# Performance work log

Measured on AMD Instinct MI355X. Metric: run time of the kernel, lower is better.

## Reference

```python
import jax, jax.numpy as jnp
import numpy as np

B, S, D, H = 4, 2048, 256, 8
HD = D // H
SCALE = float(np.sqrt(HD))  # temperature = head_dim ** 0.5


def setup_inputs() -> dict:
    key = jax.random.key(0)
    ks = jax.random.split(key, 12)
    w = lambda k, shape: jax.random.normal(k, shape, dtype=jnp.float32) * 0.05
    x = jax.random.normal(ks[0], (B, S, D), dtype=jnp.float32)
    adj = jax.random.randint(ks[1], (B, S, S), 0, 2, dtype=jnp.int32)
    return {
        "x": x,
        "adj": adj,
        "w_qkv": w(ks[2], (3 * D, D)),
        "b_qkv": jnp.zeros((3 * D,), jnp.float32),
        "ln_g": jnp.ones((D,), jnp.float32),
        "ln_b": jnp.zeros((D,), jnp.float32),
        "w_fc": w(ks[3], (D, D)),
        "b_fc": jnp.zeros((D,), jnp.float32),
        "w_z": w(ks[4], (D, D)),
        "b_z": jnp.full((D,), -2.0, jnp.float32),  # init_bias fills w_z bias with -2
        "u_z": w(ks[5], (D, D)),
        "w_r": w(ks[6], (D, D)),
        "u_r": w(ks[7], (D, D)),
        "w_g": w(ks[8], (D, D)),
        "u_g": w(ks[9], (D, D)),
    }


def reference(x, adj, w_qkv, b_qkv, ln_g, ln_b, w_fc, b_fc,
              w_z, b_z, u_z, w_r, u_r, w_g, u_g):
    residual = x
    # LayerNorm (eps=1e-5, torch default)
    mu = jnp.mean(x, axis=-1, keepdims=True)
    var = jnp.var(x, axis=-1, keepdims=True)
    xn = (x - mu) / jnp.sqrt(var + 1e-5) * ln_g + ln_b
    # fused QKV projection -> (B*H, S, 3*HD), batch-major over (b, h)
    qkv = xn @ w_qkv.T + b_qkv                       # [B,S,3D]
    qkv = qkv.reshape(B, S, H, 3 * HD).transpose(0, 2, 1, 3).reshape(B * H, S, 3 * HD)
    q, k, v = jnp.split(qkv, 3, axis=-1)
    # masked scaled dot-product attention (full NxN scores, as in original)
    attn = jnp.einsum('nqd,nkd->nqk', q, k) / SCALE  # [B*H,S,S]
    adj_r = jnp.repeat(adj, H, axis=0)               # batch-major, matches attn layout
    attn = jnp.where(adj_r == 0, -jnp.inf, attn)
    attn = jax.nn.softmax(attn, axis=-1)
    out = jnp.einsum('nqk,nkd->nqd', attn, v)        # [B*H,S,HD]
    # Faithful replication of torch's view(n_head, batch, ...) applied to
    # batch-major data (an ordering quirk in the original module).
    out = out.reshape(H, B, S, HD).transpose(1, 2, 0, 3).reshape(B, S, D)
    y = jax.nn.relu(out @ w_fc.T + b_fc)
    # GRU gate: x=residual, y=attention branch
    z = jax.nn.sigmoid(y @ w_z.T + b_z + residual @ u_z.T)
    r = jax.nn.sigmoid(y @ w_r.T + residual @ u_r.T)
    h_hat = jnp.tanh(y @ w_g.T + (r * residual) @ u_g.T)
    return (1.0 - z) * residual + z * h_hat
```

## Files before the change

kernel.cpp:

```cpp
#include <hip/hip_runtime.h>
#include <hip/hip_bf16.h>
#include <math.h>

#define B_  4
#define S_  2048
#define D_  256
#define H_  8
#define HD_ 32
#define QSCALE 0.25504175929589786f

typedef short  bf16x8 __attribute__((ext_vector_type(8)));
typedef float  f32x4  __attribute__((ext_vector_type(4)));
typedef float  f32x16 __attribute__((ext_vector_type(16)));
typedef unsigned short ushort_t;
typedef unsigned int   uint_t;

__device__ __forceinline__ ushort_t f2b(float f) {
    union { float f; unsigned u; } v; v.f = f;
    unsigned r = (v.u + 0x7FFFu + ((v.u >> 16) & 1u)) >> 16;
    return (ushort_t)r;
}
__device__ __forceinline__ float b2f(ushort_t s) {
    return __uint_as_float((uint_t)s << 16);
}
__device__ __forceinline__ f32x16 zero16() {
    f32x16 z;
#pragma unroll
    for (int i = 0; i < 16; ++i) z[i] = 0.f;
    return z;
}

__device__ __forceinline__ float wave_sum(float v) {
#pragma unroll
    for (int o = 32; o > 0; o >>= 1) v += __shfl_down(v, o, 64);
    return v;
}
__device__ __forceinline__ float block_sum256(float v, float* scr) {
    v = wave_sum(v);
    int lane = threadIdx.x & 63, wid = threadIdx.x >> 6;
    if (lane == 0) scr[wid] = v;
    __syncthreads();
    float r = scr[0] + scr[1] + scr[2] + scr[3];
    __syncthreads();
    return r;
}

#define WQ_SZ 196608
#define WS_SZ 65536
#define NB_ADJ 8192
#define NB_WC  2560
#define NB_LN  8192
__global__ __launch_bounds__(256)
void prep_kernel(const int* __restrict__ adj, uint_t* __restrict__ bits,
                 const float* __restrict__ w0, const float* __restrict__ w1,
                 const float* __restrict__ w2, const float* __restrict__ w3,
                 const float* __restrict__ w4, const float* __restrict__ w5,
                 const float* __restrict__ w6, const float* __restrict__ w7,
                 ushort_t* __restrict__ wout,
                 const float* __restrict__ x, const float* __restrict__ g,
                 const float* __restrict__ bb, ushort_t* __restrict__ xn_b) {
    __shared__ float scr[4];
    int blk = blockIdx.x, tid = threadIdx.x;
    if (blk < NB_ADJ) {
        int lane = tid & 63;
        int b = blk >> 11, q = blk & 2047;
        uint_t* outp = bits + ((size_t)b * 64) * 2048 + q;
#pragma unroll
        for (int gp = 0; gp < 8; ++gp) {
            size_t i = ((size_t)blk * 8 + gp) * 256 + tid;
            unsigned long long m = __ballot(adj[i] != 0);
            int w = gp * 8 + ((tid & ~63) >> 5);
            if (lane == 0)  outp[(size_t)w * 2048]       = (uint_t)m;
            if (lane == 32) outp[(size_t)(w + 1) * 2048] = (uint_t)(m >> 32);
        }
    } else if (blk < NB_ADJ + NB_WC) {
        int idx = (blk - NB_ADJ) * 256 + tid;
        const float* src; int o;
        if (idx < WQ_SZ) { src = w0; o = idx; }
        else {
            int j = idx - WQ_SZ, seg = j >> 16; o = j & (WS_SZ - 1);
            src = (seg == 0) ? w1 : (seg == 1) ? w2 : (seg == 2) ? w3 :
                  (seg == 3) ? w4 : (seg == 4) ? w5 : (seg == 5) ? w6 : w7;
        }
        int j  = o & 7;
        int l  = (o >> 3) & 15;
        int qd = (o >> 7) & 3;
        int ks = (o >> 9) & 7;
        int ct = o >> 12;
        wout[idx] = f2b(src[(ct * 16 + l) * 256 + ks * 32 + qd * 8 + j]);
    } else {
        size_t base = (size_t)(blk - NB_ADJ - NB_WC) * D_;
        float v  = x[base + tid];
        float mu = block_sum256(v, scr) * (1.0f / D_);
        float d  = v - mu;
        float var = block_sum256(d * d, scr) * (1.0f / D_);
        float rstd = rsqrtf(var + 1e-5f);
        xn_b[base + tid] = f2b(d * rstd * g[tid] + bb[tid]);
    }
}

__global__ __launch_bounds__(256)
void gemm_qkv(const ushort_t* __restrict__ A, const ushort_t* __restrict__ Wf,
              const float* __restrict__ bias, ushort_t* __restrict__ outb,
              ushort_t* __restrict__ vT, ushort_t* __restrict__ kD) {
    __shared__ ushort_t Sa[64][264];
    int tid = threadIdx.x;
    int wave = tid >> 6, lane = tid & 63, l = lane & 15, quad = lane >> 4;
    int wm = wave >> 1, wn = wave & 1;
    int m0 = blockIdx.y * 64, n0 = blockIdx.x * 64;
    {
#pragma unroll
        for (int j = 0; j < 8; ++j) {
            int u = tid + j * 256;
            int row = u >> 5, c = (u & 31) * 8;
            *(uint4*)&Sa[row][c] = *(const uint4*)(A + (size_t)(m0 + row) * 256 + c);
        }
    }
    __syncthreads();

    bf16x8 af[2][8];
#pragma unroll
    for (int mt = 0; mt < 2; ++mt)
#pragma unroll
        for (int ks = 0; ks < 8; ++ks)
            af[mt][ks] = *(const bf16x8*)&Sa[wm * 32 + mt * 16 + l][ks * 32 + quad * 8];

    f32x4 acc[2][2];
#pragma unroll
    for (int i = 0; i < 2; ++i)
#pragma unroll
        for (int j = 0; j < 2; ++j) acc[i][j] = (f32x4){0.f, 0.f, 0.f, 0.f};

#pragma unroll
    for (int nt = 0; nt < 2; ++nt) {
        int ct = (n0 >> 4) + wn * 2 + nt;
        bf16x8 wfr[8];
#pragma unroll
        for (int ks = 0; ks < 8; ++ks)
            wfr[ks] = *(const bf16x8*)(Wf + (((size_t)ct * 8 + ks) * 64 + lane) * 8);
#pragma unroll
        for (int ks = 0; ks < 8; ++ks) {
            acc[0][nt] = __builtin_amdgcn_mfma_f32_16x16x32_bf16(af[0][ks], wfr[ks], acc[0][nt], 0, 0, 0);
            acc[1][nt] = __builtin_amdgcn_mfma_f32_16x16x32_bf16(af[1][ks], wfr[ks], acc[1][nt], 0, 0, 0);
        }
    }

    __syncthreads();
    ushort_t* So = &Sa[0][0];
#pragma unroll
    for (int nt = 0; nt < 2; ++nt) {
        int col = wn * 32 + nt * 16 + l;
        int gcol = n0 + col;
        float bv = bias[gcol];
        float qs = ((gcol % 96) < 32) ? QSCALE : 1.0f;
#pragma unroll
        for (int mt = 0; mt < 2; ++mt)
#pragma unroll
            for (int r = 0; r < 4; ++r) {
                int row = wm * 32 + mt * 16 + quad * 4 + r;
                So[row * 72 + col] = f2b((acc[mt][nt][r] + bv) * qs);
            }
    }
    __syncthreads();
    {
        int row = tid >> 2, seg = tid & 3;
        uint4 v0 = *(uint4*)&So[row * 72 + seg * 16];
        uint4 v1 = *(uint4*)&So[row * 72 + seg * 16 + 8];
        ushort_t* op = outb + (size_t)(m0 + row) * 768 + n0 + seg * 16;
        ((uint4*)op)[0] = v0;
        ((uint4*)op)[1] = v1;
    }

    int vs = n0 % 96;

    if (vs != 64) {
        int kloc = (vs == 0) ? 32 : 0;
        int h  = (vs == 0) ? (n0 / 96) : ((n0 - 32) / 96);
        int b  = m0 >> 11;
        int s0 = m0 & (S_ - 1);
        int krow = tid >> 2, kd = (tid & 3) * 8;
        uint4 v = *(uint4*)&So[krow * 72 + kloc + kd];
        *(uint4*)&kD[((size_t)(b * 8 + h) * S_ + s0 + krow) * 32 + kd] = v;
    }

    if (vs != 0) {
        int vloc = (vs == 64) ? 0 : 32;
        int h  = (n0 + vloc) / 96;
        int b  = m0 >> 11;
        int s0 = m0 & (S_ - 1);
        ushort_t* vstage = &Sa[0][0] + 8192;
        {
            int c = tid & 31, seg = tid >> 5;
            ushort_t tmp[8];
#pragma unroll
            for (int i = 0; i < 8; ++i)
                tmp[i] = So[(seg * 8 + i) * 72 + vloc + c];
            uint_t u[4];
#pragma unroll
            for (int i = 0; i < 4; ++i)
                u[i] = (uint_t)tmp[2 * i] | ((uint_t)tmp[2 * i + 1] << 16);
            *(uint4*)&vstage[c * 72 + seg * 8] = make_uint4(u[0], u[1], u[2], u[3]);
        }
        __syncthreads();
        {
            int d = tid >> 3, tseg = tid & 7;
            uint4 v = *(uint4*)&vstage[d * 72 + tseg * 8];
            *(uint4*)&vT[((size_t)(b * 8 + h) * 32 + d) * S_ + s0 + tseg * 8] = v;
        }
    }
}

__global__ __launch_bounds__(512)
void fused_gate(const ushort_t* __restrict__ attn_b, const float* __restrict__ xf,
                const ushort_t* __restrict__ wfc, const ushort_t* __restrict__ wz,
                const ushort_t* __restrict__ uz, const ushort_t* __restrict__ wr,
                const ushort_t* __restrict__ ur, const ushort_t* __restrict__ wg,
                const ushort_t* __restrict__ ug, const float* __restrict__ bfc,
                const float* __restrict__ bz, float* __restrict__ out) {
    __shared__ ushort_t Sa[16][264];
    __shared__ ushort_t Sx[16][264];
    __shared__ ushort_t Sy[16][264];
    __shared__ ushort_t St[16][264];
    int tid = threadIdx.x;
    int wave = tid >> 6, lane = tid & 63, l = lane & 15, quad = lane >> 4;
    int m0 = blockIdx.x * 16;
    int colbase = wave * 32;

    {
        int row = tid >> 5, c0 = (tid & 31) * 8;
        const ushort_t* ap = attn_b + (size_t)(m0 + row) * 256 + c0;
        *(uint4*)&Sa[row][c0] = *((const uint4*)ap);
        const float4* xp = (const float4*)(xf + (size_t)(m0 + row) * 256 + c0);
        float4 f0 = xp[0], f1 = xp[1];
        union { __hip_bfloat162 h[4]; uint4 u; } p0;
        p0.h[0] = __float22bfloat162_rn(make_float2(f0.x, f0.y));
        p0.h[1] = __float22bfloat162_rn(make_float2(f0.z, f0.w));
        p0.h[2] = __float22bfloat162_rn(make_float2(f1.x, f1.y));
        p0.h[3] = __float22bfloat162_rn(make_float2(f1.z, f1.w));
        *(uint4*)&Sx[row][c0] = p0.u;
    }
    __syncthreads();

    {
        bf16x8 af[8];
#pragma unroll
        for (int ks = 0; ks < 8; ++ks)
            af[ks] = *(const bf16x8*)&Sa[l][ks * 32 + quad * 8];
        f32x4 ya[2];
#pragma unroll
        for (int nt = 0; nt < 2; ++nt) ya[nt] = (f32x4){0.f, 0.f, 0.f, 0.f};
#pragma unroll
        for (int nt = 0; nt < 2; ++nt) {
            size_t fb = ((size_t)(wave * 2 + nt) * 8) * 512 + lane * 8;
#pragma unroll
            for (int ks = 0; ks < 8; ++ks) {
                bf16x8 wfr = *(const bf16x8*)(wfc + fb + ks * 512);
                ya[nt] = __builtin_amdgcn_mfma_f32_16x16x32_bf16(af[ks], wfr, ya[nt], 0, 0, 0);
            }
        }
#pragma unroll
        for (int nt = 0; nt < 2; ++nt) {
            int col = colbase + nt * 16 + l;
            float bv = bfc[col];
#pragma unroll
            for (int r = 0; r < 4; ++r)
                Sy[quad * 4 + r][col] = f2b(fmaxf(ya[nt][r] + bv, 0.0f));
        }
    }
    __syncthreads();

    f32x4 az[2], ar[2], ag[2];
#pragma unroll
    for (int nt = 0; nt < 2; ++nt) {
        az[nt] = (f32x4){0.f, 0.f, 0.f, 0.f};
        ar[nt] = (f32x4){0.f, 0.f, 0.f, 0.f};
        ag[nt] = (f32x4){0.f, 0.f, 0.f, 0.f};
    }
#pragma unroll
    for (int nt = 0; nt < 2; ++nt) {
        size_t fb = ((size_t)(wave * 2 + nt) * 8) * 512 + lane * 8;
#pragma unroll
        for (int ks = 0; ks < 8; ++ks) {
            bf16x8 fy = *(const bf16x8*)&Sy[l][ks * 32 + quad * 8];
            bf16x8 fx = *(const bf16x8*)&Sx[l][ks * 32 + quad * 8];
            bf16x8 fz  = *(const bf16x8*)(wz + fb + ks * 512);
            bf16x8 fuz = *(const bf16x8*)(uz + fb + ks * 512);
            bf16x8 fr  = *(const bf16x8*)(wr + fb + ks * 512);
            bf16x8 fur = *(const bf16x8*)(ur + fb + ks * 512);
            bf16x8 fg  = *(const bf16x8*)(wg + fb + ks * 512);
            az[nt] = __builtin_amdgcn_mfma_f32_16x16x32_bf16(fy, fz,  az[nt], 0, 0, 0);
            az[nt] = __builtin_amdgcn_mfma_f32_16x16x32_bf16(fx, fuz, az[nt], 0, 0, 0);
            ar[nt] = __builtin_amdgcn_mfma_f32_16x16x32_bf16(fy, fr,  ar[nt], 0, 0, 0);
            ar[nt] = __builtin_amdgcn_mfma_f32_16x16x32_bf16(fx, fur, ar[nt], 0, 0, 0);
            ag[nt] = __builtin_amdgcn_mfma_f32_16x16x32_bf16(fy, fg,  ag[nt], 0, 0, 0);
        }
    }
#pragma unroll
    for (int nt = 0; nt < 2; ++nt) {
        int col = colbase + nt * 16 + l;
        float bzv = bz[col];
#pragma unroll
        for (int r = 0; r < 4; ++r) {
            int row = quad * 4 + r;
            az[nt][r] = 1.0f / (1.0f + __expf(-(az[nt][r] + bzv)));
            float rr  = 1.0f / (1.0f + __expf(-ar[nt][r]));
            St[row][col] = f2b(rr * b2f(Sx[row][col]));
        }
    }
    __syncthreads();

    f32x4 fcc[2];
#pragma unroll
    for (int nt = 0; nt < 2; ++nt) fcc[nt] = (f32x4){0.f, 0.f, 0.f, 0.f};
#pragma unroll
    for (int nt = 0; nt < 2; ++nt) {
        size_t fb = ((size_t)(wave * 2 + nt) * 8) * 512 + lane * 8;
#pragma unroll
        for (int ks = 0; ks < 8; ++ks) {
            bf16x8 ft = *(const bf16x8*)&St[l][ks * 32 + quad * 8];
            bf16x8 fu = *(const bf16x8*)(ug + fb + ks * 512);
            fcc[nt] = __builtin_amdgcn_mfma_f32_16x16x32_bf16(ft, fu, fcc[nt], 0, 0, 0);
        }
    }
#pragma unroll
    for (int nt = 0; nt < 2; ++nt) {
        int col = colbase + nt * 16 + l;
#pragma unroll
        for (int r = 0; r < 4; ++r) {
            int row = quad * 4 + r;
            float v = ag[nt][r] + fcc[nt][r];
            float e = __expf(2.0f * v);
            float h = 1.0f - 2.0f / (e + 1.0f);
            float zz = az[nt][r];
            size_t idx = (size_t)(m0 + row) * 256 + col;
            out[idx] = (1.0f - zz) * xf[idx] + zz * h;
        }
    }
}

__global__ __launch_bounds__(256)
void attn_kernel(const ushort_t* __restrict__ qkvb, const ushort_t* __restrict__ kD,
                 const ushort_t* __restrict__ vT,
                 const uint_t* __restrict__ abits, ushort_t* __restrict__ attn_b) {
    __shared__ ushort_t Ks[2][128][40];
    __shared__ ushort_t Vt[2][32][136];

    int tid = threadIdx.x;
    int wave = tid >> 6, lane = tid & 63;
    int lane5 = lane & 31, hi = lane >> 5;
    int hsh8 = hi * 8;
    int pair = wave >> 1, half = wave & 1;

    int lid = blockIdx.y * 32 + blockIdx.x;
    int L   = (lid & 7) * 128 + (lid >> 3);
    int q0  = (L & 31) * 64;
    int n   = L >> 5;
    int b = n >> 3, h = n & 7;
    int bp = n & 3, hp = n >> 2;

    const ushort_t* base = qkvb + (size_t)b * S_ * 768 + h * 96;
    int qbase = pair * 32;
    int myq = q0 + qbase + lane5;
    const int kofs = half * 64;

    bf16x8 qf1 = *(const bf16x8*)(base + (size_t)myq * 768 + hsh8);
    bf16x8 qf2 = *(const bf16x8*)(base + (size_t)myq * 768 + 16 + hsh8);

    bf16x8 ones;
#pragma unroll
    for (int i = 0; i < 8; ++i) ones[i] = (short)0x3F80;

    f32x16 oacc = zero16(), aones = zero16();

    int skey = tid >> 1, sj = tid & 1;
    int prow = (skey & ~12) | ((skey & 4) << 1) | ((skey & 8) >> 1);
    int pxor = ((prow >> 3) & 1) << 3;
    int vd = tid >> 3, vk = (tid & 7) * 8;
    const ushort_t* vptr = vT + ((size_t)n * 32 + vd) * S_ + vk;
    const ushort_t* kpt  = kD + ((size_t)n * S_ + skey) * 32 + sj * 16;
    const uint_t* tb = abits + ((size_t)b * 64) * 2048 + myq;

    uint_t aw0 = tb[(size_t)(half * 2 + 0) * 2048];
    uint_t aw1 = tb[(size_t)(half * 2 + 1) * 2048];
    {
        uint4 ka = *(const uint4*)(kpt);
        uint4 kb_ = *(const uint4*)(kpt + 8);
        uint4 va = *(const uint4*)(vptr);
        uint4 vb_ = *(const uint4*)(vptr + 64);
        *(uint4*)&Ks[0][prow][(sj * 16 + 0) ^ pxor] = ka;
        *(uint4*)&Ks[0][prow][(sj * 16 + 8) ^ pxor] = kb_;
        *(uint4*)&Vt[0][vd][vk] = va;
        *(uint4*)&Vt[0][vd][vk + 64] = vb_;
    }
    uint4 kv0 = *(const uint4*)(kpt + (size_t)128 * 32);
    uint4 kv1 = *(const uint4*)(kpt + (size_t)128 * 32 + 8);
    uint4 vv0 = *(const uint4*)(vptr + 128);
    uint4 vv1 = *(const uint4*)(vptr + 192);
    __syncthreads();

    int b3 = (lane >> 3) & 1;

    for (int k0 = 0; k0 < S_; k0 += 128) {
        int cur = (k0 >> 7) & 1;
        bool more = (k0 + 128 < S_);
        uint_t awn0, awn1;
        if (more) {
            *(uint4*)&Ks[cur ^ 1][prow][(sj * 16 + 0) ^ pxor] = kv0;
            *(uint4*)&Ks[cur ^ 1][prow][(sj * 16 + 8) ^ pxor] = kv1;
            *(uint4*)&Vt[cur ^ 1][vd][vk] = vv0;
            *(uint4*)&Vt[cur ^ 1][vd][vk + 64] = vv1;
            int wn = ((k0 + 128) >> 5) + half * 2;
            awn0 = tb[(size_t)(wn + 0) * 2048];
            awn1 = tb[(size_t)(wn + 1) * 2048];
            if (k0 + 256 < S_) {
                kv0 = *(const uint4*)(kpt + (size_t)(k0 + 256) * 32);
                kv1 = *(const uint4*)(kpt + (size_t)(k0 + 256) * 32 + 8);
                vv0 = *(const uint4*)(vptr + k0 + 256);
                vv1 = *(const uint4*)(vptr + k0 + 320);
            }
        }

#pragma unroll
        for (int kb2 = 0; kb2 < 2; ++kb2) {
            const int kb = kofs + kb2 * 32;
            bf16x8 kf1 = *(const bf16x8*)&Ks[cur][kb + lane5][(hi ^ b3) * 8];
            bf16x8 kf2 = *(const bf16x8*)&Ks[cur][kb + lane5][((2 + hi) ^ b3) * 8];
            f32x16 sc = zero16();
            sc = __builtin_amdgcn_mfma_f32_32x32x16_bf16(kf1, qf1, sc, 0, 0, 0);
            sc = __builtin_amdgcn_mfma_f32_32x32x16_bf16(kf2, qf2, sc, 0, 0, 0);

            uint_t wsub = (kb2 ? aw1 : aw0) >> hsh8;
            union { uint_t u[8]; bf16x8 v[2]; } pp;
#pragma unroll
            for (int i = 0; i < 8; ++i) {
                const int c = 2 * i + ((i >> 2) * 8);
                float e0 = __builtin_amdgcn_exp2f(sc[2 * i]);
                float e1 = __builtin_amdgcn_exp2f(sc[2 * i + 1]);
                uint_t m0 = (uint_t)((int)(wsub << (31 - c)) >> 31);
                uint_t m1 = (uint_t)((int)(wsub << (30 - c)) >> 31);
                e0 = __uint_as_float(__float_as_uint(e0) & m0);
                e1 = __uint_as_float(__float_as_uint(e1) & m1);
                union { __hip_bfloat162 b2; uint_t u; } p;
                p.b2 = __float22bfloat162_rn(make_float2(e0, e1));
                pp.u[i] = p.u;
            }

            bf16x8 vb1 = *(const bf16x8*)&Vt[cur][lane5][kb + hsh8];
            bf16x8 vb2 = *(const bf16x8*)&Vt[cur][lane5][kb + 16 + hsh8];

            __builtin_amdgcn_s_setprio(1);
            oacc  = __builtin_amdgcn_mfma_f32_32x32x16_bf16(pp.v[0], vb1,  oacc,  0, 0, 0);
            aones = __builtin_amdgcn_mfma_f32_32x32x16_bf16(pp.v[0], ones, aones, 0, 0, 0);
            oacc  = __builtin_amdgcn_mfma_f32_32x32x16_bf16(pp.v[1], vb2,  oacc,  0, 0, 0);
            aones = __builtin_amdgcn_mfma_f32_32x32x16_bf16(pp.v[1], ones, aones, 0, 0, 0);
            __builtin_amdgcn_s_setprio(0);
        }

        if (more) { aw0 = awn0; aw1 = awn1; }
        __syncthreads();
    }

    float* red = (float*)&Ks[0][0][0];
    if (half) {
        float* dst = red + pair * 2048 + lane * 4;
#pragma unroll
        for (int j = 0; j < 4; ++j) {
            f32x4 t;
            t[0] = oacc[4 * j]; t[1] = oacc[4 * j + 1];
            t[2] = oacc[4 * j + 2]; t[3] = oacc[4 * j + 3];
            *(f32x4*)(dst + j * 256) = t;
        }
#pragma unroll
        for (int j = 0; j < 4; ++j) {
            f32x4 t;
            t[0] = aones[4 * j]; t[1] = aones[4 * j + 1];
            t[2] = aones[4 * j + 2]; t[3] = aones[4 * j + 3];
            *(f32x4*)(dst + (4 + j) * 256) = t;
        }
    }
    __syncthreads();
    if (!half) {
        const float* src = red + pair * 2048 + lane * 4;
#pragma unroll
        for (int j = 0; j < 4; ++j) {
            f32x4 t = *(const f32x4*)(src + j * 256);
            oacc[4 * j] += t[0]; oacc[4 * j + 1] += t[1];
            oacc[4 * j + 2] += t[2]; oacc[4 * j + 3] += t[3];
        }
#pragma unroll
        for (int j = 0; j < 4; ++j) {
            f32x4 t = *(const f32x4*)(src + (4 + j) * 256);
            aones[4 * j] += t[0]; aones[4 * j + 1] += t[1];
            aones[4 * j + 2] += t[2]; aones[4 * j + 3] += t[3];
        }
    }
    __syncthreads();

    ushort_t* Ost = &Ks[0][0][0];
    if (!half) {
#pragma unroll
        for (int r = 0; r < 16; ++r) {
            int qr = (r & 3) + 8 * (r >> 2) + 4 * hi;
            Ost[(qbase + qr) * 40 + lane5] = f2b(oacc[r] / aones[r]);
        }
    }
    __syncthreads();
    {
        int row = tid >> 2, part = tid & 3;
        uint4 v = *(uint4*)&Ost[row * 40 + part * 8];
        *(uint4*)&attn_b[((size_t)(bp * S_ + q0 + row)) * 256 + hp * 32 + part * 8] = v;
    }
}

extern "C" void kernel_launch(void* const* d_in, const int* in_sizes, int n_in,
                              void* d_out, int out_size, void* d_ws, size_t ws_size,
                              hipStream_t stream) {
    const float* x     = (const float*)d_in[0];
    const int*   adj   = (const int*)d_in[1];
    const float* w_qkv = (const float*)d_in[2];
    const float* b_qkv = (const float*)d_in[3];
    const float* ln_g  = (const float*)d_in[4];
    const float* ln_b  = (const float*)d_in[5];
    const float* w_fc  = (const float*)d_in[6];
    const float* b_fc  = (const float*)d_in[7];
    const float* w_z   = (const float*)d_in[8];
    const float* b_z   = (const float*)d_in[9];
    const float* u_z   = (const float*)d_in[10];
    const float* w_r   = (const float*)d_in[11];
    const float* u_r   = (const float*)d_in[12];
    const float* w_g   = (const float*)d_in[13];
    const float* u_g   = (const float*)d_in[14];
    float* out = (float*)d_out;

    const size_t TOK  = (size_t)B_ * S_;
    const size_t TOKD = TOK * D_;
    ushort_t* xn_b   = (ushort_t*)d_ws;
    ushort_t* qkv_b  = xn_b + TOKD;
    ushort_t* attn_b = qkv_b + TOK * 768;
    ushort_t* wb     = attn_b + TOKD;
    uint_t*   bits   = (uint_t*)(wb + WQ_SZ + 7 * WS_SZ);
    ushort_t* vTb    = (ushort_t*)(bits + (size_t)B_ * S_ * S_ / 32);
    ushort_t* kDb    = vTb + (size_t)32 * 32 * S_;

    ushort_t* wq_b  = wb;
    ushort_t* wfc_b = wb + WQ_SZ;
    ushort_t* wz_b  = wfc_b + WS_SZ;
    ushort_t* uz_b  = wz_b + WS_SZ;
    ushort_t* wr_b  = uz_b + WS_SZ;
    ushort_t* ur_b  = wr_b + WS_SZ;
    ushort_t* wg_b  = ur_b + WS_SZ;
    ushort_t* ug_b  = wg_b + WS_SZ;

    prep_kernel<<<NB_ADJ + NB_WC + NB_LN, 256, 0, stream>>>(
        adj, bits, w_qkv, w_fc, w_z, u_z, w_r, u_r, w_g, u_g, wb,
        x, ln_g, ln_b, xn_b);

    gemm_qkv<<<dim3(12, 128), 256, 0, stream>>>(xn_b, wq_b, b_qkv, qkv_b, vTb, kDb);

    attn_kernel<<<dim3(S_ / 64, B_ * H_), 256, 0, stream>>>(qkv_b, kDb, vTb, bits, attn_b);

    fused_gate<<<512, 512, 0, stream>>>(
        attn_b, x, wfc_b, wz_b, uz_b, wr_b, ur_b, wg_b, ug_b, b_fc, b_z, out);
}
```

Baseline: 223.6 us.

## Overlap adjacency bitpacking with QKV GEMM and rework LayerNorm and attention loop

Moves the adjacency-to-bitmask packing out of the prep kernel and interleaves it with the QKV GEMM blocks (16 adj blocks per 3 GEMM tiles in one launch), so the bandwidth-bound adj read runs alongside the compute-bound GEMM. LayerNorm now handles one row per wave with float4 loads and xor-shuffle reductions, which removes the shared-memory block reductions and the syncs that went with them. The attention main loop is restructured into 15 unconditional iterations plus a peeled final compute step, with prefetch addresses wrapped to drop the branches. The peeled loop issues one redundant, wrapped prefetch, and the GEMM tiles now depend on the new block interleave mapping.

```diff
diff --git a/kernel.cpp b/kernel.cpp
--- a/kernel.cpp
+++ b/kernel.cpp
@@ -29,52 +29,27 @@
     for (int i = 0; i < 16; ++i) z[i] = 0.f;
     return z;
 }
-
-__device__ __forceinline__ float wave_sum(float v) {
-#pragma unroll
-    for (int o = 32; o > 0; o >>= 1) v += __shfl_down(v, o, 64);
+__device__ __forceinline__ float wave_allsum(float v) {
+#pragma unroll
+    for (int o = 32; o > 0; o >>= 1) v += __shfl_xor(v, o, 64);
     return v;
-}
-__device__ __forceinline__ float block_sum256(float v, float* scr) {
-    v = wave_sum(v);
-    int lane = threadIdx.x & 63, wid = threadIdx.x >> 6;
-    if (lane == 0) scr[wid] = v;
-    __syncthreads();
-    float r = scr[0] + scr[1] + scr[2] + scr[3];
-    __syncthreads();
-    return r;
 }
 
 #define WQ_SZ 196608
 #define WS_SZ 65536
-#define NB_ADJ 8192
 #define NB_WC  2560
-#define NB_LN  8192
+#define NB_LN4 2048
 __global__ __launch_bounds__(256)
-void prep_kernel(const int* __restrict__ adj, uint_t* __restrict__ bits,
-                 const float* __restrict__ w0, const float* __restrict__ w1,
+void prep_kernel(const float* __restrict__ w0, const float* __restrict__ w1,
                  const float* __restrict__ w2, const float* __restrict__ w3,
                  const float* __restrict__ w4, const float* __restrict__ w5,
                  const float* __restrict__ w6, const float* __restrict__ w7,
                  ushort_t* __restrict__ wout,
                  const float* __restrict__ x, const float* __restrict__ g,
                  const float* __restrict__ bb, ushort_t* __restrict__ xn_b) {
-    __shared__ float scr[4];
     int blk = blockIdx.x, tid = threadIdx.x;
-    if (blk < NB_ADJ) {
-        int lane = tid & 63;
-        int b = blk >> 11, q = blk & 2047;
-        uint_t* outp = bits + ((size_t)b * 64) * 2048 + q;
-#pragma unroll
-        for (int gp = 0; gp < 8; ++gp) {
-            size_t i = ((size_t)blk * 8 + gp) * 256 + tid;
-            unsigned long long m = __ballot(adj[i] != 0);
-            int w = gp * 8 + ((tid & ~63) >> 5);
-            if (lane == 0)  outp[(size_t)w * 2048]       = (uint_t)m;
-            if (lane == 32) outp[(size_t)(w + 1) * 2048] = (uint_t)(m >> 32);
-        }
-    } else if (blk < NB_ADJ + NB_WC) {
-        int idx = (blk - NB_ADJ) * 256 + tid;
+    if (blk < NB_WC) {
+        int idx = blk * 256 + tid;
         const float* src; int o;
         if (idx < WQ_SZ) { src = w0; o = idx; }
         else {
@@ -89,25 +64,54 @@
         int ct = o >> 12;
         wout[idx] = f2b(src[(ct * 16 + l) * 256 + ks * 32 + qd * 8 + j]);
     } else {
-        size_t base = (size_t)(blk - NB_ADJ - NB_WC) * D_;
-        float v  = x[base + tid];
-        float mu = block_sum256(v, scr) * (1.0f / D_);
-        float d  = v - mu;
-        float var = block_sum256(d * d, scr) * (1.0f / D_);
-        float rstd = rsqrtf(var + 1e-5f);
-        xn_b[base + tid] = f2b(d * rstd * g[tid] + bb[tid]);
+        int wave = tid >> 6, lane = tid & 63;
+        int row = (blk - NB_WC) * 4 + wave;
+        int col = lane * 4;
+        float4 t = *(const float4*)(x + (size_t)row * 256 + col);
+        float s = wave_allsum(t.x + t.y + t.z + t.w);
+        float mu = s * (1.0f / D_);
+        float d0 = t.x - mu, d1 = t.y - mu, d2 = t.z - mu, d3 = t.w - mu;
+        float v = wave_allsum(d0 * d0 + d1 * d1 + d2 * d2 + d3 * d3);
+        float rstd = rsqrtf(v * (1.0f / D_) + 1e-5f);
+        float4 gv = *(const float4*)(g + col);
+        float4 bv = *(const float4*)(bb + col);
+        union { ushort_t u[4]; uint2 q; } o;
+        o.u[0] = f2b(d0 * rstd * gv.x + bv.x);
+        o.u[1] = f2b(d1 * rstd * gv.y + bv.y);
+        o.u[2] = f2b(d2 * rstd * gv.z + bv.z);
+        o.u[3] = f2b(d3 * rstd * gv.w + bv.w);
+        *(uint2*)(xn_b + (size_t)row * 256 + col) = o.q;
     }
 }
 
 __global__ __launch_bounds__(256)
 void gemm_qkv(const ushort_t* __restrict__ A, const ushort_t* __restrict__ Wf,
               const float* __restrict__ bias, ushort_t* __restrict__ outb,
-              ushort_t* __restrict__ vT, ushort_t* __restrict__ kD) {
+              ushort_t* __restrict__ vT, ushort_t* __restrict__ kD,
+              const int* __restrict__ adj, uint_t* __restrict__ bits) {
     __shared__ ushort_t Sa[64][264];
     int tid = threadIdx.x;
+    int bid = blockIdx.x;
+    int grp = bid / 19, r = bid - grp * 19;
+    if (r >= 3) {
+        int a = grp * 16 + (r - 3);
+        int lane = tid & 63;
+        uint_t* outp = bits + ((size_t)(a >> 11) * 64) * 2048 + (a & 2047);
+#pragma unroll
+        for (int gp = 0; gp < 8; ++gp) {
+            size_t i = ((size_t)a * 8 + gp) * 256 + tid;
+            unsigned long long m = __ballot(adj[i] != 0);
+            int w = gp * 8 + ((tid & ~63) >> 5);
+            if (lane == 0)  outp[(size_t)w * 2048]       = (uint_t)m;
+            if (lane == 32) outp[(size_t)(w + 1) * 2048] = (uint_t)(m >> 32);
+        }
+        return;
+    }
+    int gidx = grp * 3 + r;
+    int m0 = (gidx / 12) * 64, n0 = (gidx % 12) * 64;
+
     int wave = tid >> 6, lane = tid & 63, l = lane & 15, quad = lane >> 4;
     int wm = wave >> 1, wn = wave & 1;
-    int m0 = blockIdx.y * 64, n0 = blockIdx.x * 64;
     {
 #pragma unroll
         for (int j = 0; j < 8; ++j) {
@@ -156,9 +160,9 @@
 #pragma unroll
         for (int mt = 0; mt < 2; ++mt)
 #pragma unroll
-            for (int r = 0; r < 4; ++r) {
-                int row = wm * 32 + mt * 16 + quad * 4 + r;
-                So[row * 72 + col] = f2b((acc[mt][nt][r] + bv) * qs);
+            for (int r2 = 0; r2 < 4; ++r2) {
+                int row = wm * 32 + mt * 16 + quad * 4 + r2;
+                So[row * 72 + col] = f2b((acc[mt][nt][r2] + bv) * qs);
             }
     }
     __syncthreads();
@@ -338,6 +342,42 @@
     }
 }
 
+#define ATTN_COMPUTE(CUR, A0, A1)                                                         \
+    {                                                                                     \
+        _Pragma("unroll")                                                                 \
+        for (int kb2 = 0; kb2 < 2; ++kb2) {                                               \
+            const int kb = kofs + kb2 * 32;                                               \
+            bf16x8 kf1 = *(const bf16x8*)&Ks[CUR][kb + lane5][(hi ^ b3) * 8];             \
+            bf16x8 kf2 = *(const bf16x8*)&Ks[CUR][kb + lane5][((2 + hi) ^ b3) * 8];       \
+            f32x16 sc = zero16();                                                         \
+            sc = __builtin_amdgcn_mfma_f32_32x32x16_bf16(kf1, qf1, sc, 0, 0, 0);          \
+            sc = __builtin_amdgcn_mfma_f32_32x32x16_bf16(kf2, qf2, sc, 0, 0, 0);          \
+            uint_t wsub = (kb2 ? (A1) : (A0)) >> hsh8;                                    \
+            union { uint_t u[8]; bf16x8 v[2]; } pp;                                       \
+            _Pragma("unroll")                                                             \
+            for (int i = 0; i < 8; ++i) {                                                 \
+                const int c = 2 * i + ((i >> 2) * 8);                                     \
+                float e0 = __builtin_amdgcn_exp2f(sc[2 * i]);                             \
+                float e1 = __builtin_amdgcn_exp2f(sc[2 * i + 1]);                         \
+                uint_t mm0 = (uint_t)((int)(wsub << (31 - c)) >> 31);                     \
+                uint_t mm1 = (uint_t)((int)(wsub << (30 - c)) >> 31);                     \
+                e0 = __uint_as_float(__float_as_uint(e0) & mm0);                          \
+                e1 = __uint_as_float(__float_as_uint(e1) & mm1);                          \
+                union { __hip_bfloat162 b2; uint_t u; } p;                                \
+                p.b2 = __float22bfloat162_rn(make_float2(e0, e1));                        \
+                pp.u[i] = p.u;                                                            \
+            }                                                                             \
+            bf16x8 vb1 = *(const bf16x8*)&Vt[CUR][lane5][kb + hsh8];                      \
+            bf16x8 vb2 = *(const bf16x8*)&Vt[CUR][lane5][kb + 16 + hsh8];                 \
+            __builtin_amdgcn_s_setprio(1);                                                \
+            oacc  = __builtin_amdgcn_mfma_f32_32x32x16_bf16(pp.v[0], vb1,  oacc,  0, 0, 0); \
+            aones = __builtin_amdgcn_mfma_f32_32x32x16_bf16(pp.v[0], ones, aones, 0, 0, 0); \
+            oacc  = __builtin_amdgcn_mfma_f32_32x32x16_bf16(pp.v[1], vb2,  oacc,  0, 0, 0); \
+            aones = __builtin_amdgcn_mfma_f32_32x32x16_bf16(pp.v[1], ones, aones, 0, 0, 0); \
+            __builtin_amdgcn_s_setprio(0);                                                \
+        }                                                                                 \
+    }
+
 __global__ __launch_bounds__(256)
 void attn_kernel(const ushort_t* __restrict__ qkvb, const ushort_t* __restrict__ kD,
                  const ushort_t* __restrict__ vT,
@@ -400,65 +440,30 @@
 
     int b3 = (lane >> 3) & 1;
 
-    for (int k0 = 0; k0 < S_; k0 += 128) {
-        int cur = (k0 >> 7) & 1;
-        bool more = (k0 + 128 < S_);
-        uint_t awn0, awn1;
-        if (more) {
-            *(uint4*)&Ks[cur ^ 1][prow][(sj * 16 + 0) ^ pxor] = kv0;
-            *(uint4*)&Ks[cur ^ 1][prow][(sj * 16 + 8) ^ pxor] = kv1;
-            *(uint4*)&Vt[cur ^ 1][vd][vk] = vv0;
-            *(uint4*)&Vt[cur ^ 1][vd][vk + 64] = vv1;
-            int wn = ((k0 + 128) >> 5) + half * 2;
-            awn0 = tb[(size_t)(wn + 0) * 2048];
-            awn1 = tb[(size_t)(wn + 1) * 2048];
-            if (k0 + 256 < S_) {
-                kv0 = *(const uint4*)(kpt + (size_t)(k0 + 256) * 32);
-                kv1 = *(const uint4*)(kpt + (size_t)(k0 + 256) * 32 + 8);
-                vv0 = *(const uint4*)(vptr + k0 + 256);
-                vv1 = *(const uint4*)(vptr + k0 + 320);
-            }
-        }
-
-#pragma unroll
-        for (int kb2 = 0; kb2 < 2; ++kb2) {
-            const int kb = kofs + kb2 * 32;
-            bf16x8 kf1 = *(const bf16x8*)&Ks[cur][kb + lane5][(hi ^ b3) * 8];
-            bf16x8 kf2 = *(const bf16x8*)&Ks[cur][kb + lane5][((2 + hi) ^ b3) * 8];
-            f32x16 sc = zero16();
-            sc = __builtin_amdgcn_mfma_f32_32x32x16_bf16(kf1, qf1, sc, 0, 0, 0);
-            sc = __builtin_amdgcn_mfma_f32_32x32x16_bf16(kf2, qf2, sc, 0, 0, 0);
-
-            uint_t wsub = (kb2 ? aw1 : aw0) >> hsh8;
-            union { uint_t u[8]; bf16x8 v[2]; } pp;
-#pragma unroll
-            for (int i = 0; i < 8; ++i) {
-                const int c = 2 * i + ((i >> 2) * 8);
-                float e0 = __builtin_amdgcn_exp2f(sc[2 * i]);
-                float e1 = __builtin_amdgcn_exp2f(sc[2 * i + 1]);
-                uint_t m0 = (uint_t)((int)(wsub << (31 - c)) >> 31);
-                uint_t m1 = (uint_t)((int)(wsub << (30 - c)) >> 31);
-                e0 = __uint_as_float(__float_as_uint(e0) & m0);
-                e1 = __uint_as_float(__float_as_uint(e1) & m1);
-                union { __hip_bfloat162 b2; uint_t u; } p;
-                p.b2 = __float22bfloat162_rn(make_float2(e0, e1));
-                pp.u[i] = p.u;
-            }
-
-            bf16x8 vb1 = *(const bf16x8*)&Vt[cur][lane5][kb + hsh8];
-            bf16x8 vb2 = *(const bf16x8*)&Vt[cur][lane5][kb + 16 + hsh8];
-
-            __builtin_amdgcn_s_setprio(1);
-            oacc  = __builtin_amdgcn_mfma_f32_32x32x16_bf16(pp.v[0], vb1,  oacc,  0, 0, 0);
-            aones = __builtin_amdgcn_mfma_f32_32x32x16_bf16(pp.v[0], ones, aones, 0, 0, 0);
-            oacc  = __builtin_amdgcn_mfma_f32_32x32x16_bf16(pp.v[1], vb2,  oacc,  0, 0, 0);
-            aones = __builtin_amdgcn_mfma_f32_32x32x16_bf16(pp.v[1], ones, aones, 0, 0, 0);
-            __builtin_amdgcn_s_setprio(0);
-        }
-
-        if (more) { aw0 = awn0; aw1 = awn1; }
+#pragma unroll 1
+    for (int w = 0; w < 15; ++w) {
+        int k0 = w * 128;
+        int cur = w & 1;
+        *(uint4*)&Ks[cur ^ 1][prow][(sj * 16 + 0) ^ pxor] = kv0;
+        *(uint4*)&Ks[cur ^ 1][prow][(sj * 16 + 8) ^ pxor] = kv1;
+        *(uint4*)&Vt[cur ^ 1][vd][vk] = vv0;
+        *(uint4*)&Vt[cur ^ 1][vd][vk + 64] = vv1;
+        int wn = ((k0 + 128) >> 5) + half * 2;
+        uint_t awn0 = tb[(size_t)(wn + 0) * 2048];
+        uint_t awn1 = tb[(size_t)(wn + 1) * 2048];
+        int kpre = (k0 + 256) & (S_ - 1);
+        kv0 = *(const uint4*)(kpt + (size_t)kpre * 32);
+        kv1 = *(const uint4*)(kpt + (size_t)kpre * 32 + 8);
+        vv0 = *(const uint4*)(vptr + kpre);
+        vv1 = *(const uint4*)(vptr + kpre + 64);
+
+        ATTN_COMPUTE(cur, aw0, aw1)
+
+        aw0 = awn0; aw1 = awn1;
         __syncthreads();
     }
+    ATTN_COMPUTE(1, aw0, aw1)
+    __syncthreads();
 
     float* red = (float*)&Ks[0][0][0];
     if (half) {
@@ -551,11 +556,11 @@
     ushort_t* wg_b  = ur_b + WS_SZ;
     ushort_t* ug_b  = wg_b + WS_SZ;
 
-    prep_kernel<<<NB_ADJ + NB_WC + NB_LN, 256, 0, stream>>>(
-        adj, bits, w_qkv, w_fc, w_z, u_z, w_r, u_r, w_g, u_g, wb,
+    prep_kernel<<<NB_WC + NB_LN4, 256, 0, stream>>>(
+        w_qkv, w_fc, w_z, u_z, w_r, u_r, w_g, u_g, wb,
         x, ln_g, ln_b, xn_b);
 
-    gemm_qkv<<<dim3(12, 128), 256, 0, stream>>>(xn_b, wq_b, b_qkv, qkv_b, vTb, kDb);
+    gemm_qkv<<<9728, 256, 0, stream>>>(xn_b, wq_b, b_qkv, qkv_b, vTb, kDb, adj, bits);
 
     attn_kernel<<<dim3(S_ / 64, B_ * H_), 256, 0, stream>>>(qkv_b, kDb, vTb, bits, attn_b);
 
```

After: 234.6 us. 4.9% more time.
